# Kernel optimization log

Hardware: AMD Instinct MI355X
Metric: run time of the kernel (lower is better)

Reference implementation:

```python
import jax, jax.numpy as jnp
import numpy as np

LN_EPS = 1e-5


def setup_inputs() -> dict:
    key = jax.random.key(0)
    k0, k1, k2, k3 = jax.random.split(key, 4)
    B, L, D = 8, 2048, 512
    x = jax.random.normal(k0, (B, L, D), dtype=jnp.float32)
    adj = jax.random.uniform(k1, (B, L, L), dtype=jnp.float32)  # non-negative dense adjacency
    pad_mask = jax.random.randint(k2, (B, L), 0, 2).astype(bool)  # True = padding position
    # learned params (dropout is identity in eval mode)
    W = jax.random.normal(k3, (D, D), dtype=jnp.float32) / np.sqrt(D)  # nn.Linear weight [out,in]
    b = jnp.zeros((D,), dtype=jnp.float32)
    ln_w = jnp.ones((D,), dtype=jnp.float32)
    ln_b = jnp.zeros((D,), dtype=jnp.float32)
    edge_weight = jnp.ones((1,), dtype=jnp.float32)
    return {"x": x, "adj": adj, "pad_mask": pad_mask, "W": W, "b": b,
            "ln_w": ln_w, "ln_b": ln_b, "edge_weight": edge_weight}


def reference(x, adj, pad_mask, W, b, ln_w, ln_b, edge_weight):
    B, L, D = x.shape
    # mask padded rows/cols, then add self-loops
    valid = (~pad_mask).astype(x.dtype)                      # [B,L]
    a = adj * valid[:, :, None] * valid[:, None, :]          # [B,L,L]
    a = a + jnp.eye(L, dtype=a.dtype)[None]
    # sym normalization D^{-1/2} A D^{-1/2} as elementwise row/col scaling
    deg = a.sum(-1)                                          # [B,L], >= 1 due to self-loops
    safe = jnp.where(deg > 0, deg, 1.0)
    dis = jnp.where(deg > 0, safe ** -0.5, 0.0)              # inf -> 0 per torch code
    a = dis[:, :, None] * a * dis[:, None, :]
    # learnable scalar edge weight, aggregate, linear, relu (dropout = identity in eval)
    agg = edge_weight[0] * jnp.einsum('blm,bmd->bld', a, x)  # [B,L,D]
    out = jax.nn.relu(agg @ W.T + b)
    out = out * (D ** -0.5)
    # residual + layernorm
    h = x + out
    mu = h.mean(-1, keepdims=True)
    var = ((h - mu) ** 2).mean(-1, keepdims=True)
    return ln_w * (h - mu) / jnp.sqrt(var + LN_EPS) + ln_b
```

## Files before the change

kernel.cpp:

```cpp
#include <hip/hip_runtime.h>

#define LN_EPS 1e-5f

typedef __attribute__((ext_vector_type(8))) short s16x8;
typedef __attribute__((ext_vector_type(4))) float f32x4;
typedef long long i64b;

__device__ inline unsigned int pk_bf16(float a, float b) {
    unsigned ua = __builtin_bit_cast(unsigned, a);
    unsigned ub = __builtin_bit_cast(unsigned, b);
    ua += 0x7fffu + ((ua >> 16) & 1u);
    ub += 0x7fffu + ((ub >> 16) & 1u);
    return (ua >> 16) | (ub & 0xffff0000u);
}
__device__ inline unsigned short cv_bf16(float a) {
    unsigned ua = __builtin_bit_cast(unsigned, a);
    ua += 0x7fffu + ((ua >> 16) & 1u);
    return (unsigned short)(ua >> 16);
}
__device__ inline float bf2f(unsigned short h) {
    unsigned u = ((unsigned)h) << 16;
    return __builtin_bit_cast(float, u);
}
__device__ inline unsigned pk2_fp8(float a, float b) {
    return (unsigned)__builtin_amdgcn_cvt_pk_fp8_f32(a, b, 0, false) & 0xffffu;
}
__device__ inline unsigned char cv_fp8(float a) {
    return (unsigned char)((unsigned)__builtin_amdgcn_cvt_pk_fp8_f32(a, 0.f, 0, false) & 0xffu);
}
__device__ inline void gl_lds16(const void* g, void* l) {
    __builtin_amdgcn_global_load_lds((const __attribute__((address_space(1))) void*)g,
                                     (__attribute__((address_space(3))) void*)l, 16, 0, 0);
}

__global__ __launch_bounds__(256) void k_scan(const int* __restrict__ pm,
                                              unsigned short* __restrict__ pos,
                                              unsigned short* __restrict__ idx,
                                              int* __restrict__ cnt, int L) {
    int b = blockIdx.x, t = threadIdx.x;
    const int* pmb = pm + (size_t)b * L;
    int j0 = t * 8;
    int v[8]; int s = 0;
    #pragma unroll
    for (int k = 0; k < 8; ++k) { v[k] = (pmb[j0 + k] == 0) ? 1 : 0; s += v[k]; }
    __shared__ int ps[256];
    ps[t] = s;
    __syncthreads();
    for (int off = 1; off < 256; off <<= 1) {
        int val = (t >= off) ? ps[t - off] : 0;
        __syncthreads();
        ps[t] += val;
        __syncthreads();
    }
    int base = ps[t] - s;
    unsigned short* posb = pos + (size_t)b * L;
    unsigned short* idxb = idx + (size_t)b * L;
    #pragma unroll
    for (int k = 0; k < 8; ++k) {
        posb[j0 + k] = (unsigned short)base;
        if (v[k]) { idxb[base] = (unsigned short)(j0 + k); base++; }
    }
    if (t == 255) cnt[b] = ps[255];
}

__global__ __launch_bounds__(256) void k_degxb(const float* __restrict__ adj,
                                               const int* __restrict__ pm,
                                               const float* __restrict__ ew,
                                               const float* __restrict__ W,
                                               const unsigned short* __restrict__ pos,
                                               const int* __restrict__ cnt,
                                               float* __restrict__ dis_o,
                                               float* __restrict__ rs,
                                               float* __restrict__ rself,
                                               unsigned char* __restrict__ amc8,
                                               const float* __restrict__ x,
                                               unsigned short* __restrict__ xb,
                                               unsigned short* __restrict__ aggh,
                                               unsigned short* __restrict__ Wh,
                                               int L, int nd, int nx) {
    const int D = 512;
    int bid = blockIdx.x;
    int t = threadIdx.x;
    float e = ew[0];
    if (bid >= nd) {
        int sub = bid - nd;
        if (sub >= nx) {
            int i = ((sub - nx) * 256 + t) * 16;
            #pragma unroll
            for (int k = 0; k < 16; k += 4) {
                float4 v = *(const float4*)(W + i + k);
                uint2 o;
                o.x = pk_bf16(v.x, v.y);
                o.y = pk_bf16(v.z, v.w);
                *(uint2*)(Wh + i + k) = o;
            }
            return;
        }
        int gid = sub * 256 + t;
        int row = gid >> 6;
        int co = (gid & 63) << 3;
        const float* xp = x + (size_t)row * D + co;
        float4 v0 = *(const float4*)(xp);
        float4 v1 = *(const float4*)(xp + 4);
        uint4 o;
        o.x = pk_bf16(v0.x, v0.y);
        o.y = pk_bf16(v0.z, v0.w);
        o.z = pk_bf16(v1.x, v1.y);
        o.w = pk_bf16(v1.z, v1.w);
        *(uint4*)(xb + (size_t)row * D + co) = o;
        if (pm[row] != 0) {
            uint4 oa;
            oa.x = pk_bf16(e * v0.x, e * v0.y);
            oa.y = pk_bf16(e * v0.z, e * v0.w);
            oa.z = pk_bf16(e * v1.x, e * v1.y);
            oa.w = pk_bf16(e * v1.z, e * v1.w);
            *(uint4*)(aggh + (size_t)row * D + co) = oa;
        }
        return;
    }
    int row = bid;
    int b = row / L;
    int i = row - b * L;
    const int* pmb = pm + (size_t)b * L;
    if (pmb[i] != 0) {
        if (t == 0) { dis_o[row] = 1.f; rs[row] = 0.f; rself[row] = e; }
        return;
    }
    __shared__ __align__(16) unsigned char ls8[2048 + 16];
    __shared__ float wsum[4];
    const float* arow = adj + (size_t)row * L;
    const unsigned short* posb = pos + (size_t)b * L;
    int rloc = posb[i];
    int cb = cnt[b];
    int kcap = (cb + 63) & ~63;

    for (int k = cb + t; k < kcap; k += 256) ls8[k] = 0;

    int j0 = t * 8;
    float4 a0 = *(const float4*)(arow + j0);
    float4 a1 = *(const float4*)(arow + j0 + 4);
    int4 p0 = *(const int4*)(pmb + j0);
    int4 p1 = *(const int4*)(pmb + j0 + 4);
    uint4 pv = *(const uint4*)(posb + j0);
    unsigned pc0 = pv.x & 0xffffu, pc1 = pv.x >> 16;
    unsigned pc2 = pv.y & 0xffffu, pc3 = pv.y >> 16;
    unsigned pc4 = pv.z & 0xffffu, pc5 = pv.z >> 16;
    unsigned pc6 = pv.w & 0xffffu, pc7 = pv.w >> 16;
    float m0 = p0.x == 0 ? a0.x : 0.f;
    float m1 = p0.y == 0 ? a0.y : 0.f;
    float m2 = p0.z == 0 ? a0.z : 0.f;
    float m3 = p0.w == 0 ? a0.w : 0.f;
    float m4 = p1.x == 0 ? a1.x : 0.f;
    float m5 = p1.y == 0 ? a1.y : 0.f;
    float m6 = p1.z == 0 ? a1.z : 0.f;
    float m7 = p1.w == 0 ? a1.w : 0.f;
    float s = ((m0 + m1) + (m2 + m3)) + ((m4 + m5) + (m6 + m7));
    if (p0.x == 0) ls8[pc0] = cv_fp8(m0);
    if (p0.y == 0) ls8[pc1] = cv_fp8(m1);
    if (p0.z == 0) ls8[pc2] = cv_fp8(m2);
    if (p0.w == 0) ls8[pc3] = cv_fp8(m3);
    if (p1.x == 0) ls8[pc4] = cv_fp8(m4);
    if (p1.y == 0) ls8[pc5] = cv_fp8(m5);
    if (p1.z == 0) ls8[pc6] = cv_fp8(m6);
    if (p1.w == 0) ls8[pc7] = cv_fp8(m7);

    #pragma unroll
    for (int off = 32; off; off >>= 1) s += __shfl_down(s, off);
    if ((t & 63) == 0) wsum[t >> 6] = s;
    __syncthreads();

    unsigned char* amrow = amc8 + ((size_t)b * L + rloc) * L;
    int j0b = t * 8;
    if (j0b < kcap) *(uint2*)(amrow + j0b) = *(const uint2*)(ls8 + j0b);

    if (t == 0) {
        float tot = wsum[0] + wsum[1] + wsum[2] + wsum[3];
        float d = rsqrtf(1.f + tot);
        dis_o[row]  = d;
        rs[row]     = e * d;
        rself[row]  = e * d * d;
    }
}

__global__ __launch_bounds__(256) void k_yt(const float* __restrict__ x,
                                            const float* __restrict__ dis,
                                            const unsigned short* __restrict__ idx,
                                            const int* __restrict__ cnt,
                                            unsigned char* __restrict__ yc8,
                                            int L, int D) {
    int b = blockIdx.z;
    int kb = blockIdx.x << 6;
    int db = blockIdx.y << 6;
    int cb = cnt[b];
    if (kb >= cb) return;
    __shared__ float tile[64][65];
    int t = threadIdx.x;
    int kk = t >> 2, c4 = (t & 3) << 4;
    int kg = kb + kk;
    if (kg < cb) {
        int ol = idx[(size_t)b * L + kg];
        float dl = dis[(size_t)b * L + ol];
        const float* xp = x + ((size_t)b * L + ol) * D + db + c4;
        #pragma unroll
        for (int k = 0; k < 16; k += 4) {
            float4 v = *(const float4*)(xp + k);
            tile[kk][c4 + k + 0] = v.x * dl;
            tile[kk][c4 + k + 1] = v.y * dl;
            tile[kk][c4 + k + 2] = v.z * dl;
            tile[kk][c4 + k + 3] = v.w * dl;
        }
    } else {
        #pragma unroll
        for (int k = 0; k < 16; ++k) tile[kk][c4 + k] = 0.f;
    }
    __syncthreads();
    int dr = t >> 2, k0 = (t & 3) << 4;
    unsigned char* op = yc8 + ((size_t)b * D + db + dr) * L + kb + k0;
    uint4 o;
    o.x = pk2_fp8(tile[k0 + 0][dr],  tile[k0 + 1][dr])  | (pk2_fp8(tile[k0 + 2][dr],  tile[k0 + 3][dr])  << 16);
    o.y = pk2_fp8(tile[k0 + 4][dr],  tile[k0 + 5][dr])  | (pk2_fp8(tile[k0 + 6][dr],  tile[k0 + 7][dr])  << 16);
    o.z = pk2_fp8(tile[k0 + 8][dr],  tile[k0 + 9][dr])  | (pk2_fp8(tile[k0 + 10][dr], tile[k0 + 11][dr]) << 16);
    o.w = pk2_fp8(tile[k0 + 12][dr], tile[k0 + 13][dr]) | (pk2_fp8(tile[k0 + 14][dr], tile[k0 + 15][dr]) << 16);
    *(uint4*)(op) = o;
}

__global__ __launch_bounds__(256) void k_aggmm(
    const unsigned char* __restrict__ amc8,
    const unsigned char* __restrict__ yc8,
    const unsigned short* __restrict__ xb,
    const float* __restrict__ rs,
    const float* __restrict__ rself,
    const unsigned short* __restrict__ idx,
    const int* __restrict__ cnt,
    unsigned short* __restrict__ aggh,
    int L, int D)
{
    __shared__ __align__(16) unsigned char As[64 * 64];
    __shared__ __align__(16) unsigned char Bs[128 * 64];
    int bid = blockIdx.x;
    int wid = (bid & 7) * 128 + (bid >> 3);
    int b   = wid >> 7;
    int t6  = wid & 127;
    int brow = (t6 >> 2) << 6;
    int bcol = (t6 & 3) << 7;

    int Mc = cnt[b];
    if (brow >= Mc) return;
    int Kc = (Mc + 63) & ~63;

    int t = threadIdx.x;
    int lane = t & 63;
    int w = t >> 6;
    int wr = ((w >> 1) & 1) << 5;
    int wc = (w & 1) << 6;

    const unsigned char* amb = amc8 + ((size_t)b * L + brow) * L;
    const unsigned char* yb  = yc8 + ((size_t)b * D + bcol) * L;
    const unsigned short* idxb = idx + (size_t)b * L;

    int r4 = t >> 2;
    int c4 = t & 3;

    f32x4 acc[2][4];
    #pragma unroll
    for (int i = 0; i < 2; ++i)
        #pragma unroll
        for (int j = 0; j < 4; ++j)
            acc[i][j] = (f32x4){0.f, 0.f, 0.f, 0.f};

    const int lane15 = lane & 15;
    const int k8 = (lane >> 4) << 3;

    for (int kc = 0; kc < Kc; kc += 64) {
        {
            int sc = c4 ^ (r4 & 3);
            gl_lds16(amb + (size_t)r4 * L + kc + sc * 16, As + r4 * 64 + c4 * 16);
        }
        #pragma unroll
        for (int q = 0; q < 2; ++q) {
            int row = (q << 6) + r4;
            int sc = c4 ^ (row & 3);
            gl_lds16(yb + (size_t)row * L + kc + sc * 16, Bs + row * 64 + c4 * 16);
        }
        asm volatile("s_waitcnt vmcnt(0)" ::: "memory");
        __syncthreads();
        #pragma unroll
        for (int kk = 0; kk < 2; ++kk) {
            i64b af[2], bg[4];
            #pragma unroll
            for (int f = 0; f < 2; ++f) {
                int ar = wr + (f << 4) + lane15;
                af[f] = *(const i64b*)(As + ar * 64 + (((kk << 5) + k8) ^ ((ar & 3) << 4)));
            }
            #pragma unroll
            for (int f = 0; f < 4; ++f) {
                int br = wc + (f << 4) + lane15;
                bg[f] = *(const i64b*)(Bs + br * 64 + (((kk << 5) + k8) ^ ((br & 3) << 4)));
            }
            #pragma unroll
            for (int fm = 0; fm < 2; ++fm)
                #pragma unroll
                for (int fn = 0; fn < 4; ++fn)
                    acc[fm][fn] = __builtin_amdgcn_mfma_f32_16x16x32_fp8_fp8(af[fm], bg[fn], acc[fm][fn], 0, 0, 0);
        }
        __syncthreads();
    }

    int col = lane15;
    int r0 = (lane >> 4) << 2;
    size_t bL = (size_t)b * L;
    #pragma unroll
    for (int fm = 0; fm < 2; ++fm) {
        #pragma unroll
        for (int j = 0; j < 4; ++j) {
            int rcmp = brow + wr + (fm << 4) + r0 + j;
            if (rcmp < Mc) {
                int gi = idxb[rcmp];
                float rsi = rs[bL + gi];
                float rfi = rself[bL + gi];
                const unsigned short* xrow = xb + (bL + gi) * (size_t)D;
                unsigned short* orow = aggh + (bL + gi) * (size_t)D;
                #pragma unroll
                for (int fn = 0; fn < 4; ++fn) {
                    int gd = bcol + wc + (fn << 4) + col;
                    float v = rsi * acc[fm][fn][j] + rfi * bf2f(xrow[gd]);
                    orow[gd] = cv_bf16(v);
                }
            }
        }
    }
}

__global__ __launch_bounds__(256, 2) void k_linln(
    const unsigned short* __restrict__ aggh,
    const unsigned short* __restrict__ Wh,
    const float* __restrict__ bias,
    const unsigned short* __restrict__ xb,
    const float* __restrict__ lnw,
    const float* __restrict__ lnb,
    float* __restrict__ out)
{
    const int D = 512;
    __shared__ __align__(16) unsigned short As[32 * 64];
    __shared__ __align__(16) unsigned short Bs[512 * 64];
    __shared__ float psum[32][4], psq[32][4];

    int i0 = blockIdx.x << 5;
    int t = threadIdx.x;
    int lane = t & 63;
    int w = t >> 6;
    int wcol = w << 7;

    int srow = t >> 3;
    int chunk = t & 7;
    char* Ac = (char*)As;
    char* Bc = (char*)Bs;

    f32x4 acc[2][8];
    #pragma unroll
    for (int i = 0; i < 2; ++i)
        #pragma unroll
        for (int j = 0; j < 8; ++j)
            acc[i][j] = (f32x4){0.f, 0.f, 0.f, 0.f};

    const int lane15 = lane & 15;
    const int kbyte = (lane >> 4) << 4;
    const int swa = (lane & 7) << 4;

    for (int kc = 0; kc < D; kc += 64) {
        {
            int sc = chunk ^ (srow & 7);
            gl_lds16(aggh + (size_t)(i0 + srow) * D + kc + sc * 8, Ac + srow * 128 + chunk * 16);
        }
        #pragma unroll
        for (int q = 0; q < 16; ++q) {
            int row = srow + (q << 5);
            int sc = chunk ^ (row & 7);
            gl_lds16(Wh + (size_t)row * D + kc + sc * 8, Bc + row * 128 + chunk * 16);
        }
        asm volatile("s_waitcnt vmcnt(0)" ::: "memory");
        __syncthreads();
        #pragma unroll
        for (int kk = 0; kk < 2; ++kk) {
            s16x8 af[2], bg[8];
            #pragma unroll
            for (int f = 0; f < 2; ++f) {
                int ar = (f << 4) + lane15;
                af[f] = *(const s16x8*)(Ac + ar * 128 + (((kk << 6) + kbyte) ^ ((ar & 7) << 4)));
            }
            #pragma unroll
            for (int f = 0; f < 8; ++f) {
                int br = wcol + (f << 4) + lane15;
                bg[f] = *(const s16x8*)(Bc + br * 128 + (((kk << 6) + kbyte) ^ swa));
            }
            #pragma unroll
            for (int fm = 0; fm < 2; ++fm)
                #pragma unroll
                for (int fn = 0; fn < 8; ++fn)
                    acc[fm][fn] = __builtin_amdgcn_mfma_f32_16x16x32_bf16(af[fm], bg[fn], acc[fm][fn], 0, 0, 0);
        }
        __syncthreads();
    }

    const float scale = 0.044194173824159216f;
    float bi[8], lw[8], lb[8];
    #pragma unroll
    for (int fn = 0; fn < 8; ++fn) {
        int colg = wcol + (fn << 4) + lane15;
        bi[fn] = bias[colg];
        lw[fn] = lnw[colg];
        lb[fn] = lnb[colg];
    }
    int r0 = (lane >> 4) << 2;
    #pragma unroll
    for (int fm = 0; fm < 2; ++fm) {
        #pragma unroll
        for (int j = 0; j < 4; ++j) {
            int r = (fm << 4) + r0 + j;
            const unsigned short* xrow = xb + (size_t)(i0 + r) * D;
            float s = 0.f, q = 0.f;
            #pragma unroll
            for (int fn = 0; fn < 8; ++fn) {
                int colg = wcol + (fn << 4) + lane15;
                float v = fmaxf(acc[fm][fn][j] + bi[fn], 0.f) * scale + bf2f(xrow[colg]);
                acc[fm][fn][j] = v;
                s += v;
                q += v * v;
            }
            #pragma unroll
            for (int m = 1; m < 16; m <<= 1) {
                s += __shfl_xor(s, m);
                q += __shfl_xor(q, m);
            }
            if (lane15 == 0) { psum[r][w] = s; psq[r][w] = q; }
        }
    }
    __syncthreads();
    #pragma unroll
    for (int fm = 0; fm < 2; ++fm) {
        #pragma unroll
        for (int j = 0; j < 4; ++j) {
            int r = (fm << 4) + r0 + j;
            float s = psum[r][0] + psum[r][1] + psum[r][2] + psum[r][3];
            float q = psq[r][0] + psq[r][1] + psq[r][2] + psq[r][3];
            float mu = s * (1.f / 512.f);
            float var = q * (1.f / 512.f) - mu * mu;
            float rstd = rsqrtf(var + LN_EPS);
            float* orow = out + (size_t)(i0 + r) * D;
            #pragma unroll
            for (int fn = 0; fn < 8; ++fn) {
                int colg = wcol + (fn << 4) + lane15;
                orow[colg] = lw[fn] * (acc[fm][fn][j] - mu) * rstd + lb[fn];
            }
        }
    }
}

extern "C" void kernel_launch(void* const* d_in, const int* in_sizes, int n_in,
                              void* d_out, int out_size, void* d_ws, size_t ws_size,
                              hipStream_t stream) {
    const float* x    = (const float*)d_in[0];
    const float* adj  = (const float*)d_in[1];
    const int*   pm   = (const int*)d_in[2];
    const float* W    = (const float*)d_in[3];
    const float* bias = (const float*)d_in[4];
    const float* lnw  = (const float*)d_in[5];
    const float* lnb  = (const float*)d_in[6];
    const float* ew   = (const float*)d_in[7];

    int BL = in_sizes[2];
    int L  = in_sizes[1] / BL;
    int B  = BL / L;
    int D  = in_sizes[0] / BL;

    char* ws = (char*)d_ws;
    size_t off = 0;
    float* dis   = (float*)(ws + off); off += (size_t)BL * 4;
    float* rs    = (float*)(ws + off); off += (size_t)BL * 4;
    float* rself = (float*)(ws + off); off += (size_t)BL * 4;
    unsigned short* pos = (unsigned short*)(ws + off); off += (size_t)BL * 2;
    unsigned short* idx = (unsigned short*)(ws + off); off += (size_t)BL * 2;
    int* cnt = (int*)(ws + off); off += 64;
    unsigned char* amc8 = (unsigned char*)(ws + off); off += (size_t)BL * L;
    unsigned char* yc8  = (unsigned char*)(ws + off); off += (size_t)BL * D;
    unsigned short* Wh   = (unsigned short*)(ws + off); off += (size_t)D * D * 2;
    unsigned short* aggh = (unsigned short*)(ws + off); off += (size_t)BL * D * 2;
    unsigned short* xb   = (unsigned short*)(ws + off); off += (size_t)BL * D * 2;

    float* out = (float*)d_out;
    int nx = (BL * D) / (256 * 8);
    int nw = (D * D) / (256 * 16);

    k_scan<<<B, 256, 0, stream>>>(pm, pos, idx, cnt, L);
    k_degxb<<<BL + nx + nw, 256, 0, stream>>>(adj, pm, ew, W, pos, cnt,
                                              dis, rs, rself, amc8, x, xb, aggh, Wh, L, BL, nx);
    k_yt<<<dim3(L / 64, D / 64, B), 256, 0, stream>>>(x, dis, idx, cnt, yc8, L, D);
    k_aggmm<<<B * (L / 64) * (D / 128), 256, 0, stream>>>(amc8, yc8, xb, rs, rself, idx, cnt, aggh, L, D);
    k_linln<<<BL / 32, 256, 0, stream>>>(aggh, Wh, bias, xb, lnw, lnb, out);
}
```

Before: 96.33 us.

## Use FP8 for aggregated activations and weights in linear GEMM

Converts W and the aggregated activations to FP8 instead of BF16, and switches the linear-layer GEMM to fp8 MFMA with a reworked 64-byte-row LDS layout and swizzle. The gather kernel now reads the BF16 copy of x instead of the FP32 input, halving its read traffic. This cuts memory traffic and LDS footprint for the final GEMM but adds FP8 quantization error to the linear layer, which may hurt accuracy. The launch-bounds occupancy hint on k_linln is also removed.

```diff
diff --git a/kernel.cpp b/kernel.cpp
--- a/kernel.cpp
+++ b/kernel.cpp
@@ -75,8 +75,8 @@
                                                unsigned char* __restrict__ amc8,
                                                const float* __restrict__ x,
                                                unsigned short* __restrict__ xb,
-                                               unsigned short* __restrict__ aggh,
-                                               unsigned short* __restrict__ Wh,
+                                               unsigned char* __restrict__ agg8,
+                                               unsigned char* __restrict__ W8,
                                                int L, int nd, int nx) {
     const int D = 512;
     int bid = blockIdx.x;
@@ -86,14 +86,16 @@
         int sub = bid - nd;
         if (sub >= nx) {
             int i = ((sub - nx) * 256 + t) * 16;
-            #pragma unroll
-            for (int k = 0; k < 16; k += 4) {
-                float4 v = *(const float4*)(W + i + k);
-                uint2 o;
-                o.x = pk_bf16(v.x, v.y);
-                o.y = pk_bf16(v.z, v.w);
-                *(uint2*)(Wh + i + k) = o;
-            }
+            uint4 o;
+            float4 v0 = *(const float4*)(W + i);
+            float4 v1 = *(const float4*)(W + i + 4);
+            float4 v2 = *(const float4*)(W + i + 8);
+            float4 v3 = *(const float4*)(W + i + 12);
+            o.x = pk2_fp8(v0.x, v0.y) | (pk2_fp8(v0.z, v0.w) << 16);
+            o.y = pk2_fp8(v1.x, v1.y) | (pk2_fp8(v1.z, v1.w) << 16);
+            o.z = pk2_fp8(v2.x, v2.y) | (pk2_fp8(v2.z, v2.w) << 16);
+            o.w = pk2_fp8(v3.x, v3.y) | (pk2_fp8(v3.z, v3.w) << 16);
+            *(uint4*)(W8 + i) = o;
             return;
         }
         int gid = sub * 256 + t;
@@ -109,12 +111,10 @@
         o.w = pk_bf16(v1.z, v1.w);
         *(uint4*)(xb + (size_t)row * D + co) = o;
         if (pm[row] != 0) {
-            uint4 oa;
-            oa.x = pk_bf16(e * v0.x, e * v0.y);
-            oa.y = pk_bf16(e * v0.z, e * v0.w);
-            oa.z = pk_bf16(e * v1.x, e * v1.y);
-            oa.w = pk_bf16(e * v1.z, e * v1.w);
-            *(uint4*)(aggh + (size_t)row * D + co) = oa;
+            uint2 oa;
+            oa.x = pk2_fp8(e * v0.x, e * v0.y) | (pk2_fp8(e * v0.z, e * v0.w) << 16);
+            oa.y = pk2_fp8(e * v1.x, e * v1.y) | (pk2_fp8(e * v1.z, e * v1.w) << 16);
+            *(uint2*)(agg8 + (size_t)row * D + co) = oa;
         }
         return;
     }
@@ -182,7 +182,7 @@
     }
 }
 
-__global__ __launch_bounds__(256) void k_yt(const float* __restrict__ x,
+__global__ __launch_bounds__(256) void k_yt(const unsigned short* __restrict__ xb,
                                             const float* __restrict__ dis,
                                             const unsigned short* __restrict__ idx,
                                             const int* __restrict__ cnt,
@@ -200,14 +200,14 @@
     if (kg < cb) {
         int ol = idx[(size_t)b * L + kg];
         float dl = dis[(size_t)b * L + ol];
-        const float* xp = x + ((size_t)b * L + ol) * D + db + c4;
-        #pragma unroll
-        for (int k = 0; k < 16; k += 4) {
-            float4 v = *(const float4*)(xp + k);
-            tile[kk][c4 + k + 0] = v.x * dl;
-            tile[kk][c4 + k + 1] = v.y * dl;
-            tile[kk][c4 + k + 2] = v.z * dl;
-            tile[kk][c4 + k + 3] = v.w * dl;
+        const unsigned short* xp = xb + ((size_t)b * L + ol) * D + db + c4;
+        uint4 h0 = *(const uint4*)(xp);
+        uint4 h1 = *(const uint4*)(xp + 8);
+        unsigned hv[8] = {h0.x, h0.y, h0.z, h0.w, h1.x, h1.y, h1.z, h1.w};
+        #pragma unroll
+        for (int k = 0; k < 8; ++k) {
+            tile[kk][c4 + 2 * k + 0] = bf2f((unsigned short)(hv[k] & 0xffffu)) * dl;
+            tile[kk][c4 + 2 * k + 1] = bf2f((unsigned short)(hv[k] >> 16)) * dl;
         }
     } else {
         #pragma unroll
@@ -232,7 +232,7 @@
     const float* __restrict__ rself,
     const unsigned short* __restrict__ idx,
     const int* __restrict__ cnt,
-    unsigned short* __restrict__ aggh,
+    unsigned char* __restrict__ agg8,
     int L, int D)
 {
     __shared__ __align__(16) unsigned char As[64 * 64];
@@ -319,21 +319,21 @@
                 float rsi = rs[bL + gi];
                 float rfi = rself[bL + gi];
                 const unsigned short* xrow = xb + (bL + gi) * (size_t)D;
-                unsigned short* orow = aggh + (bL + gi) * (size_t)D;
+                unsigned char* orow = agg8 + (bL + gi) * (size_t)D;
                 #pragma unroll
                 for (int fn = 0; fn < 4; ++fn) {
                     int gd = bcol + wc + (fn << 4) + col;
                     float v = rsi * acc[fm][fn][j] + rfi * bf2f(xrow[gd]);
-                    orow[gd] = cv_bf16(v);
+                    orow[gd] = cv_fp8(v);
                 }
             }
         }
     }
 }
 
-__global__ __launch_bounds__(256, 2) void k_linln(
-    const unsigned short* __restrict__ aggh,
-    const unsigned short* __restrict__ Wh,
+__global__ __launch_bounds__(256) void k_linln(
+    const unsigned char* __restrict__ agg8,
+    const unsigned char* __restrict__ W8,
     const float* __restrict__ bias,
     const unsigned short* __restrict__ xb,
     const float* __restrict__ lnw,
@@ -341,8 +341,8 @@
     float* __restrict__ out)
 {
     const int D = 512;
-    __shared__ __align__(16) unsigned short As[32 * 64];
-    __shared__ __align__(16) unsigned short Bs[512 * 64];
+    __shared__ __align__(16) unsigned char As[32 * 64];
+    __shared__ __align__(16) unsigned char Bs[512 * 64];
     __shared__ float psum[32][4], psq[32][4];
 
     int i0 = blockIdx.x << 5;
@@ -351,10 +351,8 @@
     int w = t >> 6;
     int wcol = w << 7;
 
-    int srow = t >> 3;
-    int chunk = t & 7;
-    char* Ac = (char*)As;
-    char* Bc = (char*)Bs;
+    int r4 = t >> 2;
+    int c4 = t & 3;
 
     f32x4 acc[2][8];
     #pragma unroll
@@ -364,40 +362,40 @@
             acc[i][j] = (f32x4){0.f, 0.f, 0.f, 0.f};
 
     const int lane15 = lane & 15;
-    const int kbyte = (lane >> 4) << 4;
-    const int swa = (lane & 7) << 4;
+    const int k8 = (lane >> 4) << 3;
 
     for (int kc = 0; kc < D; kc += 64) {
-        {
-            int sc = chunk ^ (srow & 7);
-            gl_lds16(aggh + (size_t)(i0 + srow) * D + kc + sc * 8, Ac + srow * 128 + chunk * 16);
-        }
-        #pragma unroll
-        for (int q = 0; q < 16; ++q) {
-            int row = srow + (q << 5);
-            int sc = chunk ^ (row & 7);
-            gl_lds16(Wh + (size_t)row * D + kc + sc * 8, Bc + row * 128 + chunk * 16);
+        if (t < 128) {
+            int row = t >> 2;
+            int sc = c4 ^ (row & 3);
+            gl_lds16(agg8 + (size_t)(i0 + row) * D + kc + sc * 16, As + t * 16);
+        }
+        #pragma unroll
+        for (int q = 0; q < 8; ++q) {
+            int row = (q << 6) + r4;
+            int sc = c4 ^ (row & 3);
+            gl_lds16(W8 + (size_t)row * D + kc + sc * 16, Bs + row * 64 + c4 * 16);
         }
         asm volatile("s_waitcnt vmcnt(0)" ::: "memory");
         __syncthreads();
         #pragma unroll
         for (int kk = 0; kk < 2; ++kk) {
-            s16x8 af[2], bg[8];
+            i64b af[2], bg[8];
             #pragma unroll
             for (int f = 0; f < 2; ++f) {
                 int ar = (f << 4) + lane15;
-                af[f] = *(const s16x8*)(Ac + ar * 128 + (((kk << 6) + kbyte) ^ ((ar & 7) << 4)));
+                af[f] = *(const i64b*)(As + ar * 64 + (((kk << 5) + k8) ^ ((ar & 3) << 4)));
             }
             #pragma unroll
             for (int f = 0; f < 8; ++f) {
                 int br = wcol + (f << 4) + lane15;
-                bg[f] = *(const s16x8*)(Bc + br * 128 + (((kk << 6) + kbyte) ^ swa));
+                bg[f] = *(const i64b*)(Bs + br * 64 + (((kk << 5) + k8) ^ ((br & 3) << 4)));
             }
             #pragma unroll
             for (int fm = 0; fm < 2; ++fm)
                 #pragma unroll
                 for (int fn = 0; fn < 8; ++fn)
-                    acc[fm][fn] = __builtin_amdgcn_mfma_f32_16x16x32_bf16(af[fm], bg[fn], acc[fm][fn], 0, 0, 0);
+                    acc[fm][fn] = __builtin_amdgcn_mfma_f32_16x16x32_fp8_fp8(af[fm], bg[fn], acc[fm][fn], 0, 0, 0);
         }
         __syncthreads();
     }
@@ -483,9 +481,9 @@
     int* cnt = (int*)(ws + off); off += 64;
     unsigned char* amc8 = (unsigned char*)(ws + off); off += (size_t)BL * L;
     unsigned char* yc8  = (unsigned char*)(ws + off); off += (size_t)BL * D;
-    unsigned short* Wh   = (unsigned short*)(ws + off); off += (size_t)D * D * 2;
-    unsigned short* aggh = (unsigned short*)(ws + off); off += (size_t)BL * D * 2;
-    unsigned short* xb   = (unsigned short*)(ws + off); off += (size_t)BL * D * 2;
+    unsigned char* W8   = (unsigned char*)(ws + off); off += (size_t)D * D;
+    unsigned char* agg8 = (unsigned char*)(ws + off); off += (size_t)BL * D;
+    unsigned short* xb  = (unsigned short*)(ws + off); off += (size_t)BL * D * 2;
 
     float* out = (float*)d_out;
     int nx = (BL * D) / (256 * 8);
@@ -493,8 +491,8 @@
 
     k_scan<<<B, 256, 0, stream>>>(pm, pos, idx, cnt, L);
     k_degxb<<<BL + nx + nw, 256, 0, stream>>>(adj, pm, ew, W, pos, cnt,
-                                              dis, rs, rself, amc8, x, xb, aggh, Wh, L, BL, nx);
-    k_yt<<<dim3(L / 64, D / 64, B), 256, 0, stream>>>(x, dis, idx, cnt, yc8, L, D);
-    k_aggmm<<<B * (L / 64) * (D / 128), 256, 0, stream>>>(amc8, yc8, xb, rs, rself, idx, cnt, aggh, L, D);
-    k_linln<<<BL / 32, 256, 0, stream>>>(aggh, Wh, bias, xb, lnw, lnb, out);
-}
+                                              dis, rs, rself, amc8, x, xb, agg8, W8, L, BL, nx);
+    k_yt<<<dim3(L / 64, D / 64, B), 256, 0, stream>>>(xb, dis, idx, cnt, yc8, L, D);
+    k_aggmm<<<B * (L / 64) * (D / 128), 256, 0, stream>>>(amc8, yc8, xb, rs, rself, idx, cnt, agg8, L, D);
+    k_linln<<<BL / 32, 256, 0, stream>>>(agg8, W8, bias, xb, lnw, lnb, out);
+}
```

Result: faster. 84.39 us (-12.4%).
